# Optimization experiments

Measured on AMD Instinct MI355X. Metric: run time of the kernel, lower is better.

Reference implementation:

```python
import jax, jax.numpy as jnp
import numpy as np

D_MODEL = 128; D_STATE = 64; D_CONV = 4; EXPAND = 2; HEADDIM = 32; NGROUPS = 1
D_INNER = EXPAND * D_MODEL            # 256
NHEADS = D_INNER // HEADDIM           # 8
CONV_DIM = D_INNER + 2 * NGROUPS * D_STATE   # 384 (x, B, C streams)
D_IN_PROJ = 2 * D_INNER + 2 * NGROUPS * D_STATE + NHEADS  # 648 (z, xBC, dt)
EPS = 1e-5


def setup_inputs() -> dict:
    key = jax.random.key(0)
    ks = jax.random.split(key, 8)
    B, L = 8, 4096
    x = jax.random.normal(ks[0], (B, L, D_MODEL), jnp.float32)
    norm_w = jnp.ones((D_MODEL,), jnp.float32)
    in_proj_w = jax.random.normal(ks[1], (D_IN_PROJ, D_MODEL), jnp.float32) * (D_MODEL ** -0.5)
    conv_w = jax.random.normal(ks[2], (CONV_DIM, D_CONV), jnp.float32) * (D_CONV ** -0.5)
    conv_b = jnp.zeros((CONV_DIM,), jnp.float32)
    dt_bias = jax.random.uniform(ks[3], (NHEADS,), jnp.float32, -4.0, -1.0)
    A_log = jnp.log(jax.random.uniform(ks[4], (NHEADS,), jnp.float32, 1.0, 16.0))
    D = jnp.ones((NHEADS,), jnp.float32)
    gnorm_w = jnp.ones((D_INNER,), jnp.float32)
    out_proj_w = jax.random.normal(ks[5], (D_MODEL, D_INNER), jnp.float32) * (D_INNER ** -0.5)
    return dict(x=x, norm_w=norm_w, in_proj_w=in_proj_w, conv_w=conv_w, conv_b=conv_b,
                dt_bias=dt_bias, A_log=A_log, D=D, gnorm_w=gnorm_w, out_proj_w=out_proj_w)


def _rmsnorm(x, w):
    return x * jax.lax.rsqrt(jnp.mean(x * x, axis=-1, keepdims=True) + EPS) * w


def _causal_dw_conv(x, w, b):
    # x: [B,L,C]; w: [C,K]; depthwise causal conv along L
    K = w.shape[1]
    xp = jnp.pad(x, ((0, 0), (K - 1, 0), (0, 0)))
    kern = jnp.transpose(w)[:, None, :]  # [K,1,C] for WIO with groups=C
    out = jax.lax.conv_general_dilated(
        xp, kern, window_strides=(1,), padding='VALID',
        dimension_numbers=('NWC', 'WIO', 'NWC'),
        feature_group_count=w.shape[0])
    return out + b


def _ssm(xh, dt, Bm, Cm, A):
    # xh: [B,L,H,P]; dt: [B,L,H]; Bm, Cm: [B,L,N]; A: [H]
    def step(h, inp):
        x_t, dt_t, B_t, C_t = inp
        dA = jnp.exp(dt_t * A)                                   # [B,H]
        h = h * dA[..., None, None] + (dt_t[..., None] * x_t)[..., None] * B_t[:, None, None, :]
        y = jnp.einsum('bhpn,bn->bhp', h, C_t)
        return h, y
    Bsz, L, H, P = xh.shape
    N = Bm.shape[-1]
    h0 = jnp.zeros((Bsz, H, P, N), xh.dtype)
    xs = (xh.transpose(1, 0, 2, 3), dt.transpose(1, 0, 2),
          Bm.transpose(1, 0, 2), Cm.transpose(1, 0, 2))
    _, ys = jax.lax.scan(step, h0, xs)
    return ys.transpose(1, 0, 2, 3)  # [B,L,H,P]


def reference(x, norm_w, in_proj_w, conv_w, conv_b, dt_bias, A_log, D, gnorm_w, out_proj_w):
    xn = _rmsnorm(x, norm_w)
    zxbcdt = xn @ in_proj_w.T                                    # [B,L,648]
    z, xBC, dt = jnp.split(zxbcdt, [D_INNER, D_INNER + CONV_DIM], axis=-1)
    dt = jax.nn.softplus(dt + dt_bias)                           # [B,L,H]
    xBC = jax.nn.silu(_causal_dw_conv(xBC, conv_w, conv_b))
    xs, Bm, Cm = jnp.split(xBC, [D_INNER, D_INNER + NGROUPS * D_STATE], axis=-1)
    Bsz, L, _ = x.shape
    xh = xs.reshape(Bsz, L, NHEADS, HEADDIM)
    A = -jnp.exp(A_log)                                          # [H]
    y = _ssm(xh, dt, Bm, Cm, A) + D[None, None, :, None] * xh    # D skip per head
    y = y.reshape(Bsz, L, D_INNER)
    y = _rmsnorm(y * jax.nn.silu(z), gnorm_w)                    # gated RMSNorm
    out = y @ out_proj_w.T
    return x + out
```

## Files before the change

kernel.cpp:

```cpp
#include <hip/hip_runtime.h>

#define DM    128
#define DI    256
#define NH    8
#define HD    32
#define NS    64
#define CDIM  384
#define DPROJ 648
#define LSEQ  4096
#define NB    8
#define NTOK  32768
#define LC    64
#define NC    64
#define EPSF  1e-5f
#define LOG2E 1.4426950408889634f

typedef __bf16 bf16;
typedef bf16  bf16x8 __attribute__((ext_vector_type(8)));
typedef bf16  bf16x4 __attribute__((ext_vector_type(4)));
typedef short short8 __attribute__((ext_vector_type(8)));
typedef float f32x4  __attribute__((ext_vector_type(4)));

__device__ __forceinline__ unsigned short f2bfbits(float f) {
    unsigned int u = __float_as_uint(f);
    unsigned int r = u + 0x7FFFu + ((u >> 16) & 1u);
    return (unsigned short)(r >> 16);
}
__device__ __forceinline__ float bfbits2f(unsigned short u) {
    return __uint_as_float(((unsigned int)u) << 16);
}

__global__ __launch_bounds__(256) void k_prep(const float* __restrict__ w1,
                                              const float* __restrict__ w2,
                                              const float* __restrict__ gw,
                                              unsigned short* __restrict__ w1g,
                                              unsigned short* __restrict__ w2f) {
    int i = blockIdx.x * 256 + threadIdx.x;
    if (i < 640 * DM) {
        int f = i >> 9, r = i & 511;
        int lane = r >> 3, jj = r & 7;
        int ns = f >> 2, kk = f & 3;
        int n = ns * 16 + (lane & 15), k = kk * 32 + (lane >> 4) * 8 + jj;
        w1g[i] = f2bfbits(w1[(size_t)n * DM + k]);
    } else {
        int j = i - 640 * DM;
        if (j < DM * DI) {
            int f = j >> 9, r = j & 511;
            int lane = r >> 3, jj = r & 7;
            int kk = f >> 3, nt = f & 7;
            int fr = lane & 15, ko = lane >> 4;
            int n = nt * 16 + fr, k = kk * 32 + ko * 8 + jj;
            w2f[j] = f2bfbits(w2[(size_t)n * DI + k] * gw[k]);
        }
    }
}

__global__ __launch_bounds__(256, 4) void k_gemm1(const float* __restrict__ x,
                                                  const float* __restrict__ nw,
                                                  const float* __restrict__ w1,
                                                  const float* __restrict__ dtb,
                                                  const unsigned short* __restrict__ w1g,
                                                  unsigned short* __restrict__ zb,
                                                  unsigned short* __restrict__ xbc,
                                                  float* __restrict__ dtf) {
    __shared__ float Xs[64][132];
    __shared__ float Wd[8][132];
    const int t = threadIdx.x;
    const int wave = t >> 6, lane = t & 63;
    const int m0 = blockIdx.x * 64;
    const int ny = blockIdx.y;
    if (ny == 0) {
        int row = t >> 5, col = (t & 31) * 4;
        *(float4*)&Wd[row][col] = *(const float4*)(w1 + (size_t)(640 + row) * DM + col);
    }
    const float nw0 = nw[lane * 2], nw1 = nw[lane * 2 + 1];
    #pragma unroll
    for (int i = 0; i < 16; i++) {
        int r = wave * 16 + i;
        const float* xr = x + (size_t)(m0 + r) * DM + lane * 2;
        float v0 = xr[0], v1 = xr[1];
        float ss = v0 * v0 + v1 * v1;
        #pragma unroll
        for (int o = 32; o; o >>= 1) ss += __shfl_xor(ss, o);
        float rs = rsqrtf(ss * (1.0f / DM) + EPSF);
        Xs[r][lane * 2]     = v0 * rs * nw0;
        Xs[r][lane * 2 + 1] = v1 * rs * nw1;
    }
    __syncthreads();
    if (ny == 0) {
        const int h = lane >> 3, ks = lane & 7;
        const float dtbh = dtb[h];
        #pragma unroll
        for (int i = 0; i < 16; i++) {
            int r = wave * 16 + i;
            float acc = 0.f;
            #pragma unroll
            for (int q = 0; q < 4; q++) {
                float4 xv = *(const float4*)&Xs[r][ks * 16 + q * 4];
                float4 wv = *(const float4*)&Wd[h][ks * 16 + q * 4];
                acc = fmaf(xv.x, wv.x, acc); acc = fmaf(xv.y, wv.y, acc);
                acc = fmaf(xv.z, wv.z, acc); acc = fmaf(xv.w, wv.w, acc);
            }
            acc += __shfl_xor(acc, 1);
            acc += __shfl_xor(acc, 2);
            acc += __shfl_xor(acc, 4);
            if (ks == 0) {
                float v = acc + dtbh;
                dtf[(size_t)(m0 + r) * NH + h] = (v > 20.f) ? v : log1pf(expf(v));
            }
        }
    }
    const int wm = wave >> 1, wn = wave & 1;
    const int fr = lane & 15, ko = lane >> 4;
    bf16x8 a[2][4];
    #pragma unroll
    for (int mt = 0; mt < 2; mt++)
        #pragma unroll
        for (int kk = 0; kk < 4; kk++) {
            const float* src = &Xs[wm * 32 + mt * 16 + fr][kk * 32 + ko * 8];
            float4 lo = *(const float4*)src, hi = *(const float4*)(src + 4);
            bf16x8 af;
            af[0] = (bf16)lo.x; af[1] = (bf16)lo.y; af[2] = (bf16)lo.z; af[3] = (bf16)lo.w;
            af[4] = (bf16)hi.x; af[5] = (bf16)hi.y; af[6] = (bf16)hi.z; af[7] = (bf16)hi.w;
            a[mt][kk] = af;
        }
    for (int i = 0; i < 5; i++) {
        int nt = ny * 5 + i;
        const unsigned short* wb = w1g + (((size_t)(nt * 4 + wn * 2) * 4) << 9) + lane * 8;
        f32x4 acc[2][2] = {};
        #pragma unroll
        for (int kk = 0; kk < 4; kk++) {
            bf16x8 b0 = *(const bf16x8*)(wb + ((size_t)kk << 9));
            bf16x8 b1 = *(const bf16x8*)(wb + ((size_t)(4 + kk) << 9));
            acc[0][0] = __builtin_amdgcn_mfma_f32_16x16x32_bf16(a[0][kk], b0, acc[0][0], 0, 0, 0);
            acc[1][0] = __builtin_amdgcn_mfma_f32_16x16x32_bf16(a[1][kk], b0, acc[1][0], 0, 0, 0);
            acc[0][1] = __builtin_amdgcn_mfma_f32_16x16x32_bf16(a[0][kk], b1, acc[0][1], 0, 0, 0);
            acc[1][1] = __builtin_amdgcn_mfma_f32_16x16x32_bf16(a[1][kk], b1, acc[1][1], 0, 0, 0);
        }
        unsigned short* dst; int ld, nc0;
        if (nt < 4) { dst = zb;  ld = DI;   nc0 = nt * 64; }
        else        { dst = xbc; ld = CDIM; nc0 = nt * 64 - 256; }
        #pragma unroll
        for (int mt = 0; mt < 2; mt++)
            #pragma unroll
            for (int ntt = 0; ntt < 2; ntt++) {
                int n = nc0 + wn * 32 + ntt * 16 + fr;
                #pragma unroll
                for (int rr = 0; rr < 4; rr++) {
                    int m = m0 + wm * 32 + mt * 16 + ko * 4 + rr;
                    dst[(size_t)m * ld + n] = f2bfbits(acc[mt][ntt][rr]);
                }
            }
    }
}

__global__ __launch_bounds__(512) void k_conv1(const unsigned short* __restrict__ xbc,
                                               const float* __restrict__ cw,
                                               const float* __restrict__ cb,
                                               const float* __restrict__ dtf,
                                               const float* __restrict__ alog,
                                               unsigned short* __restrict__ bcA,
                                               unsigned short* __restrict__ xT,
                                               unsigned short* __restrict__ hst,
                                               float* __restrict__ dAp) {
    __shared__ __align__(16) unsigned short L[320][72];
    __shared__ float wlh[NH][64];
    const int tid = threadIdx.x;
    const int t0 = blockIdx.x * 64;
    if (tid < CDIM) {
        const int ch = tid;
        const int l0 = t0 & (LSEQ - 1);
        float4 wv = *(const float4*)(cw + ch * 4);
        float bias = cb[ch];
        const unsigned short* in = xbc + (size_t)t0 * CDIM + ch;
        float h1 = 0.f, h2 = 0.f, h3 = 0.f;
        if (l0) {
            h1 = bfbits2f(in[-CDIM]);
            h2 = bfbits2f(in[-2 * CDIM]);
            h3 = bfbits2f(in[-3 * CDIM]);
        }
        short8 pk;
        #pragma unroll 8
        for (int t = 0; t < 64; t++) {
            float x0 = bfbits2f(in[(size_t)t * CDIM]);
            float acc = bias;
            acc = fmaf(x0, wv.w, acc);
            acc = fmaf(h1, wv.z, acc);
            acc = fmaf(h2, wv.y, acc);
            acc = fmaf(h3, wv.x, acc);
            float s = acc / (1.f + expf(-acc));
            unsigned short us = f2bfbits(s);
            if (ch >= 256) bcA[(size_t)(t0 + t) * 128 + (ch - 256)] = us;
            pk[t & 7] = (short)us;
            if (ch < 320 && (t & 7) == 7) *(short8*)&L[ch][t - 7] = pk;
            h3 = h2; h2 = h1; h1 = x0;
        }
    }
    __syncthreads();
    {
        int idx = tid;
        #pragma unroll
        for (int it = 0; it < 4; it++, idx += 512) {
            int row = idx >> 3, tc = (idx & 7) * 8;
            *(short8*)(xT + (size_t)row * NTOK + t0 + tc) = *(const short8*)&L[row][tc];
        }
    }
    const int h = tid >> 6, lane = tid & 63;
    const int b = blockIdx.x >> 6, c = blockIdx.x & 63;
    const int bh = b * NH + h;
    const float A = -expf(alog[h]);
    float dt = dtf[(size_t)(t0 + lane) * NH + h];
    float q = dt * A * LOG2E;
    #pragma unroll
    for (int o = 1; o <= 32; o <<= 1) {
        float tmp = __shfl_up(q, o);
        if (lane >= o) q += tmp;
    }
    float qL = __shfl(q, 63);
    wlh[h][lane] = exp2f(qL - q) * dt;
    if (lane == 0) dAp[(size_t)bh * NC + c] = exp2f(qL);
    const int m = lane & 15, ko = lane >> 4;
    f32x4 hacc[4][2] = {};
    #pragma unroll
    for (int kh = 0; kh < 2; kh++) {
        bf16x8 xb[2];
        #pragma unroll
        for (int pi = 0; pi < 2; pi++)
            xb[pi] = *(const bf16x8*)&L[h * HD + pi * 16 + m][kh * 32 + ko * 8];
        f32x4 w0 = *(const f32x4*)&wlh[h][kh * 32 + ko * 8];
        f32x4 w1v = *(const f32x4*)&wlh[h][kh * 32 + ko * 8 + 4];
        #pragma unroll
        for (int ni = 0; ni < 4; ni++) {
            bf16x8 bv = *(const bf16x8*)&L[256 + ni * 16 + m][kh * 32 + ko * 8];
            bf16x8 af;
            #pragma unroll
            for (int j = 0; j < 4; j++) af[j] = (bf16)((float)bv[j] * w0[j]);
            #pragma unroll
            for (int j = 0; j < 4; j++) af[4 + j] = (bf16)((float)bv[4 + j] * w1v[j]);
            #pragma unroll
            for (int pi = 0; pi < 2; pi++)
                hacc[ni][pi] = __builtin_amdgcn_mfma_f32_16x16x32_bf16(af, xb[pi], hacc[ni][pi], 0, 0, 0);
        }
    }
    unsigned short* hb = hst + (((size_t)bh * NC + c) << 11);
    #pragma unroll
    for (int ni = 0; ni < 4; ni++)
        #pragma unroll
        for (int pi = 0; pi < 2; pi++) {
            bf16x4 pv;
            #pragma unroll
            for (int r = 0; r < 4; r++) pv[r] = (bf16)hacc[ni][pi][r];
            *(bf16x4*)(hb + (pi * 16 + m) * 64 + ni * 16 + ko * 4) = pv;
        }
}

__global__ __launch_bounds__(256) void k_ssm2(unsigned short* __restrict__ hst,
                                              const float* __restrict__ dAp) {
    __shared__ float dl[NC];
    const int bh = blockIdx.x >> 3, seg = blockIdx.x & 7;
    const int s = seg * 256 + threadIdx.x;
    if (threadIdx.x < NC) dl[threadIdx.x] = dAp[(size_t)bh * NC + threadIdx.x];
    __syncthreads();
    unsigned short* p = hst + ((size_t)bh * NC << 11) + s;
    float r = 0.f;
    float v0 = bfbits2f(p[0]);
    float v1 = bfbits2f(p[(size_t)1 << 11]);
    float v2 = bfbits2f(p[(size_t)2 << 11]);
    float v3 = bfbits2f(p[(size_t)3 << 11]);
    for (int c = 0; c < NC; c += 4) {
        float t;
        t = v0; if (c + 4 < NC) v0 = bfbits2f(p[(size_t)(c + 4) << 11]);
        p[(size_t)c << 11] = f2bfbits(r);       r = fmaf(r, dl[c], t);
        t = v1; if (c + 5 < NC) v1 = bfbits2f(p[(size_t)(c + 5) << 11]);
        p[(size_t)(c + 1) << 11] = f2bfbits(r); r = fmaf(r, dl[c + 1], t);
        t = v2; if (c + 6 < NC) v2 = bfbits2f(p[(size_t)(c + 6) << 11]);
        p[(size_t)(c + 2) << 11] = f2bfbits(r); r = fmaf(r, dl[c + 2], t);
        t = v3; if (c + 7 < NC) v3 = bfbits2f(p[(size_t)(c + 7) << 11]);
        p[(size_t)(c + 3) << 11] = f2bfbits(r); r = fmaf(r, dl[c + 3], t);
    }
}

__global__ __launch_bounds__(256, 2) void k_ssd3(const unsigned short* __restrict__ bcA,
                                                 const unsigned short* __restrict__ xT,
                                                 const float* __restrict__ dtf,
                                                 const float* __restrict__ alog,
                                                 const unsigned short* __restrict__ hst,
                                                 const float* __restrict__ Dw,
                                                 unsigned short* __restrict__ ybb) {
    __shared__ __align__(16) bf16 Pl[4][64 * 72];
    __shared__ __align__(16) float ql[4][64];
    __shared__ __align__(16) float dl[4][64];
    const int bh = blockIdx.x >> 4, cg = blockIdx.x & 15;
    const int b = bh >> 3, h = bh & 7;
    const int wave = threadIdx.x >> 6, lane = threadIdx.x & 63;
    const int c = cg * 4 + wave;
    const size_t tok0 = (size_t)b * LSEQ + c * LC;
    const float A = -expf(alog[h]);
    const float Dh = Dw[h];
    float dt = dtf[(tok0 + lane) * NH + h];
    float q = dt * A * LOG2E;
    #pragma unroll
    for (int o = 1; o <= 32; o <<= 1) {
        float tmp = __shfl_up(q, o);
        if (lane >= o) q += tmp;
    }
    ql[wave][lane] = q;
    dl[wave][lane] = dt;
    const int m = lane & 15, ko = lane >> 4;
    bf16x8 cf[4][2];
    #pragma unroll
    for (int ti = 0; ti < 4; ti++)
        #pragma unroll
        for (int kh = 0; kh < 2; kh++)
            cf[ti][kh] = *(const bf16x8*)(bcA + (tok0 + ti * 16 + m) * 128 + 64 + kh * 32 + ko * 8);
    f32x4 gt[4][4] = {};
    #pragma unroll
    for (int kh = 0; kh < 2; kh++) {
        bf16x8 bfg[4];
        #pragma unroll
        for (int si = 0; si < 4; si++)
            bfg[si] = *(const bf16x8*)(bcA + (tok0 + si * 16 + m) * 128 + kh * 32 + ko * 8);
        #pragma unroll
        for (int ti = 0; ti < 4; ti++)
            #pragma unroll
            for (int si = 0; si < 4; si++)
                gt[ti][si] = __builtin_amdgcn_mfma_f32_16x16x32_bf16(bfg[si], cf[ti][kh], gt[ti][si], 0, 0, 0);
    }
    float qt[4];
    #pragma unroll
    for (int ti = 0; ti < 4; ti++) qt[ti] = ql[wave][ti * 16 + m];
    #pragma unroll
    for (int si = 0; si < 4; si++) {
        f32x4 qs = *(const f32x4*)&ql[wave][si * 16 + ko * 4];
        f32x4 ds = *(const f32x4*)&dl[wave][si * 16 + ko * 4];
        #pragma unroll
        for (int ti = 0; ti < 4; ti++) {
            bf16x4 pv = {};
            if (si <= ti) {
                const int t = ti * 16 + m;
                #pragma unroll
                for (int r = 0; r < 4; r++) {
                    int s = si * 16 + ko * 4 + r;
                    float p = 0.f;
                    if (s <= t) {
                        p = exp2f(qt[ti] - qs[r]) * ds[r] * gt[ti][si][r];
                        if (s == t) p += Dh;
                    }
                    pv[r] = (bf16)p;
                }
            }
            *(bf16x4*)&Pl[wave][(ti * 16 + m) * 72 + si * 16 + ko * 4] = pv;
        }
    }
    f32x4 et[4];
    #pragma unroll
    for (int ti = 0; ti < 4; ti++) {
        f32x4 qv = *(const f32x4*)&ql[wave][ti * 16 + ko * 4];
        #pragma unroll
        for (int r = 0; r < 4; r++) et[ti][r] = exp2f(qv[r]);
    }
    const size_t hbase = ((size_t)bh * NC + c) << 11;
    f32x4 ya[4][2] = {}, ua[4][2] = {};
    #pragma unroll
    for (int kh = 0; kh < 2; kh++) {
        bf16x8 xb[2], hb2[2];
        #pragma unroll
        for (int pi = 0; pi < 2; pi++) {
            xb[pi]  = *(const bf16x8*)(xT + (size_t)(h * HD + pi * 16 + m) * NTOK + tok0 + kh * 32 + ko * 8);
            hb2[pi] = *(const bf16x8*)(hst + hbase + (pi * 16 + m) * 64 + kh * 32 + ko * 8);
        }
        #pragma unroll
        for (int ti = 0; ti < 4; ti++) {
            bf16x8 pa = *(const bf16x8*)&Pl[wave][(ti * 16 + m) * 72 + kh * 32 + ko * 8];
            #pragma unroll
            for (int pi = 0; pi < 2; pi++) {
                ya[ti][pi] = __builtin_amdgcn_mfma_f32_16x16x32_bf16(pa, xb[pi], ya[ti][pi], 0, 0, 0);
                ua[ti][pi] = __builtin_amdgcn_mfma_f32_16x16x32_bf16(cf[ti][kh], hb2[pi], ua[ti][pi], 0, 0, 0);
            }
        }
    }
    unsigned short* yrow = ybb + tok0 * DI + h * HD;
    #pragma unroll
    for (int ti = 0; ti < 4; ti++)
        #pragma unroll
        for (int pi = 0; pi < 2; pi++)
            #pragma unroll
            for (int r = 0; r < 4; r++) {
                int t = ti * 16 + ko * 4 + r;
                yrow[(size_t)t * DI + pi * 16 + m] =
                    f2bfbits(ya[ti][pi][r] + et[ti][r] * ua[ti][pi][r]);
            }
}

__global__ __launch_bounds__(256, 4) void k_gemm2g(const unsigned short* __restrict__ ybb,
                                                   const unsigned short* __restrict__ zb,
                                                   const unsigned short* __restrict__ w2f,
                                                   const float* __restrict__ xin,
                                                   float* __restrict__ out) {
    const int t = threadIdx.x;
    const int wave = t >> 6, lane = t & 63;
    const int fr = lane & 15, ko = lane >> 4;
    const int m0 = blockIdx.x * 64 + wave * 16;
    const size_t rowo = (size_t)(m0 + fr) * DI;
    float ss = 0.f;
    bf16x8 gb[8];
    #pragma unroll
    for (int kk = 0; kk < 8; kk++) {
        int co = kk * 32 + ko * 8;
        bf16x8 yv = *(const bf16x8*)(ybb + rowo + co);
        bf16x8 zv = *(const bf16x8*)(zb + rowo + co);
        #pragma unroll
        for (int j = 0; j < 8; j++) {
            float z = (float)zv[j];
            float g = (float)yv[j] * (z / (1.f + expf(-z)));
            ss += g * g;
            gb[kk][j] = (bf16)g;
        }
    }
    ss += __shfl_xor(ss, 16);
    ss += __shfl_xor(ss, 32);
    const float rs = rsqrtf(ss * (1.0f / DI) + EPSF);
    #pragma unroll
    for (int kk = 0; kk < 8; kk++)
        #pragma unroll
        for (int j = 0; j < 8; j++)
            gb[kk][j] = (bf16)((float)gb[kk][j] * rs);
    const unsigned short* wp = w2f + (size_t)lane * 8;
    f32x4 acc[8] = {};
    #pragma unroll
    for (int kk = 0; kk < 8; kk++) {
        #pragma unroll
        for (int nt = 0; nt < 8; nt++) {
            bf16x8 bfr = *(const bf16x8*)(wp + (((size_t)kk * 8 + nt) << 9));
            acc[nt] = __builtin_amdgcn_mfma_f32_16x16x32_bf16(gb[kk], bfr, acc[nt], 0, 0, 0);
        }
    }
    #pragma unroll
    for (int nt = 0; nt < 8; nt++) {
        int n = nt * 16 + fr;
        #pragma unroll
        for (int rr = 0; rr < 4; rr++) {
            int m = m0 + ko * 4 + rr;
            out[(size_t)m * DM + n] = xin[(size_t)m * DM + n] + acc[nt][rr];
        }
    }
}

extern "C" void kernel_launch(void* const* d_in, const int* in_sizes, int n_in,
                              void* d_out, int out_size, void* d_ws, size_t ws_size,
                              hipStream_t stream) {
    const float* x   = (const float*)d_in[0];
    const float* nw  = (const float*)d_in[1];
    const float* w1  = (const float*)d_in[2];
    const float* cw  = (const float*)d_in[3];
    const float* cb  = (const float*)d_in[4];
    const float* dtb = (const float*)d_in[5];
    const float* al  = (const float*)d_in[6];
    const float* Dw  = (const float*)d_in[7];
    const float* gw  = (const float*)d_in[8];
    const float* w2  = (const float*)d_in[9];
    float* out = (float*)d_out;

    float* ws = (float*)d_ws;
    float*  dAp = ws;
    float*  dtf = dAp + NB * NH * NC;
    unsigned short* hst = (unsigned short*)(dtf + (size_t)NTOK * NH);
    unsigned short* zb  = hst + (size_t)NB * NH * NC * 2048;
    unsigned short* xbc = zb + (size_t)NTOK * DI;
    unsigned short* bcA = xbc + (size_t)NTOK * CDIM;
    unsigned short* xT  = bcA + (size_t)NTOK * 128;
    unsigned short* ybb = xT + (size_t)DI * NTOK;
    unsigned short* w1g = ybb + (size_t)NTOK * DI;
    unsigned short* w2f = w1g + (size_t)640 * DM;

    k_prep<<<(640 * DM + DM * DI + 255) / 256, 256, 0, stream>>>(w1, w2, gw, w1g, w2f);
    k_gemm1<<<dim3(NTOK / 64, 2), 256, 0, stream>>>(x, nw, w1, dtb, w1g, zb, xbc, dtf);
    k_conv1<<<NTOK / 64, 512, 0, stream>>>(xbc, cw, cb, dtf, al, bcA, xT, hst, dAp);
    k_ssm2<<<NB * NH * 8, 256, 0, stream>>>(hst, dAp);
    k_ssd3<<<NB * NH * (NC / 4), 256, 0, stream>>>(bcA, xT, dtf, al, hst, Dw, ybb);
    k_gemm2g<<<NTOK / 64, 256, 0, stream>>>(ybb, zb, w2f, x, out);
}
```

Measured before the change: 189.1 us.

## Fuse SSD chunk kernel with gated RMSNorm and output projection

Merges the intra-chunk SSD kernel and the gated-norm/out-projection GEMM into one kernel. Each block now handles one 64-token chunk across all 8 heads (512 threads), stages B/C in shared memory, and keeps the y tile in LDS instead of writing it to global memory and reading it back. The G matrix is computed in two halves to cut register pressure. The goal is to drop one launch plus the bf16 y round trip through HBM, at the cost of larger LDS use, extra block barriers and fewer blocks in flight.

```diff
diff --git a/kernel.cpp b/kernel.cpp
--- a/kernel.cpp
+++ b/kernel.cpp
@@ -280,21 +280,35 @@
     }
 }
 
-__global__ __launch_bounds__(256, 2) void k_ssd3(const unsigned short* __restrict__ bcA,
-                                                 const unsigned short* __restrict__ xT,
-                                                 const float* __restrict__ dtf,
-                                                 const float* __restrict__ alog,
-                                                 const unsigned short* __restrict__ hst,
-                                                 const float* __restrict__ Dw,
-                                                 unsigned short* __restrict__ ybb) {
-    __shared__ __align__(16) bf16 Pl[4][64 * 72];
-    __shared__ __align__(16) float ql[4][64];
-    __shared__ __align__(16) float dl[4][64];
-    const int bh = blockIdx.x >> 4, cg = blockIdx.x & 15;
-    const int b = bh >> 3, h = bh & 7;
-    const int wave = threadIdx.x >> 6, lane = threadIdx.x & 63;
-    const int c = cg * 4 + wave;
-    const size_t tok0 = (size_t)b * LSEQ + c * LC;
+__global__ __launch_bounds__(512, 2) void k_ssd3g(const unsigned short* __restrict__ bcA,
+                                                  const unsigned short* __restrict__ xT,
+                                                  const float* __restrict__ dtf,
+                                                  const float* __restrict__ alog,
+                                                  const unsigned short* __restrict__ hst,
+                                                  const float* __restrict__ Dw,
+                                                  const unsigned short* __restrict__ zb,
+                                                  const unsigned short* __restrict__ w2f,
+                                                  const float* __restrict__ xin,
+                                                  float* __restrict__ out) {
+    __shared__ __align__(16) unsigned short BC[64][136];
+    __shared__ __align__(16) bf16 PlY[NH][64 * 40];
+    __shared__ float ql[NH][64];
+    __shared__ float dl[NH][64];
+    const int tid = threadIdx.x;
+    const int b = blockIdx.x >> 6, c = blockIdx.x & 63;
+    const int t0 = blockIdx.x * 64;
+    const size_t tok0 = (size_t)t0;
+    {
+        int idx = tid;
+        #pragma unroll
+        for (int it = 0; it < 2; it++, idx += 512) {
+            int tok = idx >> 4, c8 = (idx & 15) * 8;
+            *(short8*)&BC[tok][c8] = *(const short8*)(bcA + (tok0 + tok) * 128 + c8);
+        }
+    }
+    __syncthreads();
+    const int h = tid >> 6, lane = tid & 63;
+    const int bh = b * NH + h;
     const float A = -expf(alog[h]);
     const float Dh = Dw[h];
     float dt = dtf[(tok0 + lane) * NH + h];
@@ -304,144 +318,151 @@
         float tmp = __shfl_up(q, o);
         if (lane >= o) q += tmp;
     }
-    ql[wave][lane] = q;
-    dl[wave][lane] = dt;
+    ql[h][lane] = q;
+    dl[h][lane] = dt;
     const int m = lane & 15, ko = lane >> 4;
+    bf16* Pw = &PlY[h][0];
     bf16x8 cf[4][2];
     #pragma unroll
     for (int ti = 0; ti < 4; ti++)
         #pragma unroll
         for (int kh = 0; kh < 2; kh++)
-            cf[ti][kh] = *(const bf16x8*)(bcA + (tok0 + ti * 16 + m) * 128 + 64 + kh * 32 + ko * 8);
-    f32x4 gt[4][4] = {};
+            cf[ti][kh] = *(const bf16x8*)&BC[ti * 16 + m][64 + kh * 32 + ko * 8];
+    float qt[4];
+    #pragma unroll
+    for (int ti = 0; ti < 4; ti++) qt[ti] = ql[h][ti * 16 + m];
+    const size_t hbase = ((size_t)bh * NC + c) << 11;
+    f32x4 ya[4][2] = {}, ua[4][2] = {};
     #pragma unroll
     for (int kh = 0; kh < 2; kh++) {
-        bf16x8 bfg[4];
-        #pragma unroll
-        for (int si = 0; si < 4; si++)
-            bfg[si] = *(const bf16x8*)(bcA + (tok0 + si * 16 + m) * 128 + kh * 32 + ko * 8);
+        bf16x8 hb2[2];
+        #pragma unroll
+        for (int pi = 0; pi < 2; pi++)
+            hb2[pi] = *(const bf16x8*)(hst + hbase + (pi * 16 + m) * 64 + kh * 32 + ko * 8);
         #pragma unroll
         for (int ti = 0; ti < 4; ti++)
             #pragma unroll
-            for (int si = 0; si < 4; si++)
-                gt[ti][si] = __builtin_amdgcn_mfma_f32_16x16x32_bf16(bfg[si], cf[ti][kh], gt[ti][si], 0, 0, 0);
-    }
-    float qt[4];
-    #pragma unroll
-    for (int ti = 0; ti < 4; ti++) qt[ti] = ql[wave][ti * 16 + m];
-    #pragma unroll
-    for (int si = 0; si < 4; si++) {
-        f32x4 qs = *(const f32x4*)&ql[wave][si * 16 + ko * 4];
-        f32x4 ds = *(const f32x4*)&dl[wave][si * 16 + ko * 4];
+            for (int pi = 0; pi < 2; pi++)
+                ua[ti][pi] = __builtin_amdgcn_mfma_f32_16x16x32_bf16(cf[ti][kh], hb2[pi], ua[ti][pi], 0, 0, 0);
+    }
+    #pragma unroll
+    for (int sh = 0; sh < 2; sh++) {
+        f32x4 gth[4][2] = {};
+        #pragma unroll
+        for (int kh = 0; kh < 2; kh++) {
+            bf16x8 bfg[2];
+            #pragma unroll
+            for (int sj = 0; sj < 2; sj++)
+                bfg[sj] = *(const bf16x8*)&BC[(sh * 2 + sj) * 16 + m][kh * 32 + ko * 8];
+            #pragma unroll
+            for (int ti = 0; ti < 4; ti++)
+                #pragma unroll
+                for (int sj = 0; sj < 2; sj++)
+                    gth[ti][sj] = __builtin_amdgcn_mfma_f32_16x16x32_bf16(bfg[sj], cf[ti][kh], gth[ti][sj], 0, 0, 0);
+        }
+        #pragma unroll
+        for (int sj = 0; sj < 2; sj++) {
+            const int si = sh * 2 + sj;
+            f32x4 qs = *(const f32x4*)&ql[h][si * 16 + ko * 4];
+            f32x4 ds = *(const f32x4*)&dl[h][si * 16 + ko * 4];
+            #pragma unroll
+            for (int ti = 0; ti < 4; ti++) {
+                bf16x4 pv = {};
+                if (si <= ti) {
+                    const int t = ti * 16 + m;
+                    #pragma unroll
+                    for (int r = 0; r < 4; r++) {
+                        int s = si * 16 + ko * 4 + r;
+                        float p = 0.f;
+                        if (s <= t) {
+                            p = exp2f(qt[ti] - qs[r]) * ds[r] * gth[ti][sj][r];
+                            if (s == t) p += Dh;
+                        }
+                        pv[r] = (bf16)p;
+                    }
+                }
+                *(bf16x4*)&Pw[(ti * 16 + m) * 40 + sj * 16 + ko * 4] = pv;
+            }
+        }
+        bf16x8 xb[2];
+        #pragma unroll
+        for (int pi = 0; pi < 2; pi++)
+            xb[pi] = *(const bf16x8*)(xT + (size_t)(h * HD + pi * 16 + m) * NTOK + tok0 + sh * 32 + ko * 8);
         #pragma unroll
         for (int ti = 0; ti < 4; ti++) {
-            bf16x4 pv = {};
-            if (si <= ti) {
-                const int t = ti * 16 + m;
+            bf16x8 pa = *(const bf16x8*)&Pw[(ti * 16 + m) * 40 + ko * 8];
+            #pragma unroll
+            for (int pi = 0; pi < 2; pi++)
+                ya[ti][pi] = __builtin_amdgcn_mfma_f32_16x16x32_bf16(pa, xb[pi], ya[ti][pi], 0, 0, 0);
+        }
+    }
+    __syncthreads();
+    unsigned short* Ys = (unsigned short*)&PlY[0][0];
+    {
+        f32x4 et[4];
+        #pragma unroll
+        for (int ti = 0; ti < 4; ti++) {
+            f32x4 qv = *(const f32x4*)&ql[h][ti * 16 + ko * 4];
+            #pragma unroll
+            for (int r = 0; r < 4; r++) et[ti][r] = exp2f(qv[r]);
+        }
+        #pragma unroll
+        for (int ti = 0; ti < 4; ti++)
+            #pragma unroll
+            for (int pi = 0; pi < 2; pi++)
                 #pragma unroll
                 for (int r = 0; r < 4; r++) {
-                    int s = si * 16 + ko * 4 + r;
-                    float p = 0.f;
-                    if (s <= t) {
-                        p = exp2f(qt[ti] - qs[r]) * ds[r] * gt[ti][si][r];
-                        if (s == t) p += Dh;
-                    }
-                    pv[r] = (bf16)p;
+                    int t = ti * 16 + ko * 4 + r;
+                    Ys[t * 264 + h * HD + pi * 16 + m] =
+                        f2bfbits(ya[ti][pi][r] + et[ti][r] * ua[ti][pi][r]);
                 }
-            }
-            *(bf16x4*)&Pl[wave][(ti * 16 + m) * 72 + si * 16 + ko * 4] = pv;
-        }
-    }
-    f32x4 et[4];
-    #pragma unroll
-    for (int ti = 0; ti < 4; ti++) {
-        f32x4 qv = *(const f32x4*)&ql[wave][ti * 16 + ko * 4];
-        #pragma unroll
-        for (int r = 0; r < 4; r++) et[ti][r] = exp2f(qv[r]);
-    }
-    const size_t hbase = ((size_t)bh * NC + c) << 11;
-    f32x4 ya[4][2] = {}, ua[4][2] = {};
-    #pragma unroll
-    for (int kh = 0; kh < 2; kh++) {
-        bf16x8 xb[2], hb2[2];
-        #pragma unroll
-        for (int pi = 0; pi < 2; pi++) {
-            xb[pi]  = *(const bf16x8*)(xT + (size_t)(h * HD + pi * 16 + m) * NTOK + tok0 + kh * 32 + ko * 8);
-            hb2[pi] = *(const bf16x8*)(hst + hbase + (pi * 16 + m) * 64 + kh * 32 + ko * 8);
-        }
-        #pragma unroll
-        for (int ti = 0; ti < 4; ti++) {
-            bf16x8 pa = *(const bf16x8*)&Pl[wave][(ti * 16 + m) * 72 + kh * 32 + ko * 8];
-            #pragma unroll
-            for (int pi = 0; pi < 2; pi++) {
-                ya[ti][pi] = __builtin_amdgcn_mfma_f32_16x16x32_bf16(pa, xb[pi], ya[ti][pi], 0, 0, 0);
-                ua[ti][pi] = __builtin_amdgcn_mfma_f32_16x16x32_bf16(cf[ti][kh], hb2[pi], ua[ti][pi], 0, 0, 0);
-            }
-        }
-    }
-    unsigned short* yrow = ybb + tok0 * DI + h * HD;
-    #pragma unroll
-    for (int ti = 0; ti < 4; ti++)
-        #pragma unroll
-        for (int pi = 0; pi < 2; pi++)
-            #pragma unroll
-            for (int r = 0; r < 4; r++) {
-                int t = ti * 16 + ko * 4 + r;
-                yrow[(size_t)t * DI + pi * 16 + m] =
-                    f2bfbits(ya[ti][pi][r] + et[ti][r] * ua[ti][pi][r]);
-            }
-}
-
-__global__ __launch_bounds__(256, 4) void k_gemm2g(const unsigned short* __restrict__ ybb,
-                                                   const unsigned short* __restrict__ zb,
-                                                   const unsigned short* __restrict__ w2f,
-                                                   const float* __restrict__ xin,
-                                                   float* __restrict__ out) {
-    const int t = threadIdx.x;
-    const int wave = t >> 6, lane = t & 63;
-    const int fr = lane & 15, ko = lane >> 4;
-    const int m0 = blockIdx.x * 64 + wave * 16;
-    const size_t rowo = (size_t)(m0 + fr) * DI;
-    float ss = 0.f;
-    bf16x8 gb[8];
-    #pragma unroll
-    for (int kk = 0; kk < 8; kk++) {
-        int co = kk * 32 + ko * 8;
-        bf16x8 yv = *(const bf16x8*)(ybb + rowo + co);
-        bf16x8 zv = *(const bf16x8*)(zb + rowo + co);
-        #pragma unroll
-        for (int j = 0; j < 8; j++) {
-            float z = (float)zv[j];
-            float g = (float)yv[j] * (z / (1.f + expf(-z)));
-            ss += g * g;
-            gb[kk][j] = (bf16)g;
-        }
-    }
-    ss += __shfl_xor(ss, 16);
-    ss += __shfl_xor(ss, 32);
-    const float rs = rsqrtf(ss * (1.0f / DI) + EPSF);
-    #pragma unroll
-    for (int kk = 0; kk < 8; kk++)
-        #pragma unroll
-        for (int j = 0; j < 8; j++)
-            gb[kk][j] = (bf16)((float)gb[kk][j] * rs);
-    const unsigned short* wp = w2f + (size_t)lane * 8;
-    f32x4 acc[8] = {};
-    #pragma unroll
-    for (int kk = 0; kk < 8; kk++) {
-        #pragma unroll
-        for (int nt = 0; nt < 8; nt++) {
-            bf16x8 bfr = *(const bf16x8*)(wp + (((size_t)kk * 8 + nt) << 9));
-            acc[nt] = __builtin_amdgcn_mfma_f32_16x16x32_bf16(gb[kk], bfr, acc[nt], 0, 0, 0);
-        }
-    }
-    #pragma unroll
-    for (int nt = 0; nt < 8; nt++) {
-        int n = nt * 16 + fr;
-        #pragma unroll
-        for (int rr = 0; rr < 4; rr++) {
-            int m = m0 + ko * 4 + rr;
-            out[(size_t)m * DM + n] = xin[(size_t)m * DM + n] + acc[nt][rr];
+    }
+    __syncthreads();
+    {
+        const int rg = h & 3, nh = h >> 2;
+        const int r0 = rg * 16;
+        const size_t rowo = (tok0 + r0 + m) * DI;
+        float ss = 0.f;
+        bf16x8 gb[8];
+        #pragma unroll
+        for (int kk = 0; kk < 8; kk++) {
+            int co = kk * 32 + ko * 8;
+            bf16x8 yv = *(const bf16x8*)&Ys[(r0 + m) * 264 + co];
+            bf16x8 zv = *(const bf16x8*)(zb + rowo + co);
+            #pragma unroll
+            for (int j = 0; j < 8; j++) {
+                float z = (float)zv[j];
+                float g = (float)yv[j] * (z / (1.f + expf(-z)));
+                ss += g * g;
+                gb[kk][j] = (bf16)g;
+            }
+        }
+        ss += __shfl_xor(ss, 16);
+        ss += __shfl_xor(ss, 32);
+        const float rs = rsqrtf(ss * (1.0f / DI) + EPSF);
+        #pragma unroll
+        for (int kk = 0; kk < 8; kk++)
+            #pragma unroll
+            for (int j = 0; j < 8; j++)
+                gb[kk][j] = (bf16)((float)gb[kk][j] * rs);
+        const unsigned short* wp = w2f + (size_t)lane * 8;
+        f32x4 acc[4] = {};
+        #pragma unroll
+        for (int kk = 0; kk < 8; kk++) {
+            #pragma unroll
+            for (int ntl = 0; ntl < 4; ntl++) {
+                bf16x8 bfr = *(const bf16x8*)(wp + (((size_t)kk * 8 + nh * 4 + ntl) << 9));
+                acc[ntl] = __builtin_amdgcn_mfma_f32_16x16x32_bf16(gb[kk], bfr, acc[ntl], 0, 0, 0);
+            }
+        }
+        #pragma unroll
+        for (int ntl = 0; ntl < 4; ntl++) {
+            int n = (nh * 4 + ntl) * 16 + m;
+            #pragma unroll
+            for (int rr = 0; rr < 4; rr++) {
+                size_t row = tok0 + r0 + ko * 4 + rr;
+                out[row * DM + n] = xin[row * DM + n] + acc[ntl][rr];
+            }
         }
     }
 }
@@ -469,14 +490,12 @@
     unsigned short* xbc = zb + (size_t)NTOK * DI;
     unsigned short* bcA = xbc + (size_t)NTOK * CDIM;
     unsigned short* xT  = bcA + (size_t)NTOK * 128;
-    unsigned short* ybb = xT + (size_t)DI * NTOK;
-    unsigned short* w1g = ybb + (size_t)NTOK * DI;
+    unsigned short* w1g = xT + (size_t)DI * NTOK;
     unsigned short* w2f = w1g + (size_t)640 * DM;
 
     k_prep<<<(640 * DM + DM * DI + 255) / 256, 256, 0, stream>>>(w1, w2, gw, w1g, w2f);
     k_gemm1<<<dim3(NTOK / 64, 2), 256, 0, stream>>>(x, nw, w1, dtb, w1g, zb, xbc, dtf);
     k_conv1<<<NTOK / 64, 512, 0, stream>>>(xbc, cw, cb, dtf, al, bcA, xT, hst, dAp);
     k_ssm2<<<NB * NH * 8, 256, 0, stream>>>(hst, dAp);
-    k_ssd3<<<NB * NH * (NC / 4), 256, 0, stream>>>(bcA, xT, dtf, al, hst, Dw, ybb);
-    k_gemm2g<<<NTOK / 64, 256, 0, stream>>>(ybb, zb, w2f, x, out);
-}
+    k_ssd3g<<<NTOK / 64, 512, 0, stream>>>(bcA, xT, dtf, al, hst, Dw, zb, w2f, x, out);
+}
```

After: 177.0 us. -6.4%, faster.
